# Optimization experiments

Hardware: AMD Instinct MI355X
Metric: run time of the kernel (lower is better)

The kernel has to match this reference:

```python
import math
import jax, jax.numpy as jnp
import numpy as np

P = 8; K = 9; RC = 8; FC = 768; TOPK = 2
THR = 0.2; TEMP = 0.08; DIL = 5; MIX = 0.65; OPEN = 5


def _build_bank():
    axis = np.linspace(-1.0, 1.0, K, dtype=np.float32)
    yy, xx = np.meshgrid(axis, axis, indexing='ij')
    Ls = [0.45, 0.75, 1.05]; Ws = [0.14, 0.2, 0.28]
    kernels, oris, lens, wids = [], [], [], []
    for i in range(P):
        ang = 2.0 * math.pi * i / P
        L = Ls[i % 3]; W = Ws[(i // 3) % 3]
        xr = xx * math.cos(ang) + yy * math.sin(ang)
        yr = -xx * math.sin(ang) + yy * math.cos(ang)
        taper = (1.0 - np.clip(np.abs(xr) / L, 0.0, 1.0)) ** 1.5
        core = np.exp(-0.5 * ((xr / L) ** 2 + (yr / W) ** 2))
        ridge = taper * core * np.clip(1.0 - (yr / W) ** 2, 0.0, None)
        k = ridge - ridge.mean()
        k = k / max(np.abs(k).sum(), 1e-6)
        kernels.append(k.astype(np.float32)); oris.append(ang); lens.append(L); wids.append(W)
    return (jnp.asarray(np.stack(kernels)[:, None]),
            jnp.asarray(np.array(oris, np.float32)),
            jnp.asarray(np.array(lens, np.float32)),
            jnp.asarray(np.array(wids, np.float32)))


def _conv(x, w, b, pad):
    y = jax.lax.conv_general_dilated(x, w, (1, 1), [(pad, pad), (pad, pad)],
                                     dimension_numbers=('NCHW', 'OIHW', 'NCHW'))
    return y + b[None, :, None, None]


def _avg3(x):  # torch avg_pool2d k=3,s=1,p=1 with count_include_pad=True -> sum/9
    s = jax.lax.reduce_window(x, 0.0, jax.lax.add, (1, 1, 3, 3), (1, 1, 1, 1),
                              [(0, 0), (0, 0), (1, 1), (1, 1)])
    return s / 9.0


def _maxp(x, k):
    p = k // 2
    return jax.lax.reduce_window(x, -jnp.inf, jax.lax.max, (1, 1, k, k), (1, 1, 1, 1),
                                 [(0, 0), (0, 0), (p, p), (p, p)])


def _binary_open(mask, k):
    eroded = 1.0 - _maxp(1.0 - mask, k)
    return jnp.clip(_maxp(eroded, k), 0.0, 1.0)


def _normalize(t):
    mn = t.min(axis=(-2, -1), keepdims=True)
    mx = t.max(axis=(-2, -1), keepdims=True)
    return (t - mn) / jnp.maximum(mx - mn, 1e-6)


def _gelu(x):
    return jax.nn.gelu(x, approximate=False)


def _forward(feature_map, theta, length, width, curvature, alpha, objectness,
             prototype_logits, fp1_w, fp1_b, fp2_w, fp2_b, pm1_w, pm1_b,
             pm2_w, pm2_b, proto_delta):
    bank, ori, la, wa = _build_bank()
    carrier = _gelu(_conv(_gelu(_conv(feature_map, fp1_w, fp1_b, 0)), fp2_w, fp2_b, 1))
    carrier_mean = carrier.mean(axis=1, keepdims=True)
    carrier_hp = carrier_mean - _avg3(carrier_mean)
    kernels = bank + 0.05 * proto_delta
    responses = jax.lax.conv_general_dilated(carrier_hp, kernels, (1, 1),
                                             [(K // 2, K // 2)] * 2,
                                             dimension_numbers=('NCHW', 'OIHW', 'NCHW'))
    theta_angle = jnp.tanh(theta) * math.pi  # [B,1,H,W]
    theta_score = jnp.cos(theta_angle - ori[None, :, None, None])
    length_value = jax.nn.sigmoid(length) * 0.85 + 0.25
    width_value = jax.nn.sigmoid(width) * 0.22 + 0.08
    length_score = -(length_value - la[None, :, None, None]) ** 2 / 0.08
    width_score = -(width_value - wa[None, :, None, None]) ** 2 / 0.01
    bias = prototype_logits + 1.25 * theta_score + length_score + width_score
    pw = jax.nn.softmax(bias, axis=1)  # [B,P,H,W]
    # per-pixel top-k prototype selection
    pwt = jnp.moveaxis(pw, 1, -1)  # [B,H,W,P]
    vals, idx = jax.lax.top_k(pwt, TOPK)
    sparse = (jax.nn.one_hot(idx, P, dtype=pw.dtype) * vals[..., None]).sum(axis=-2)
    sparse = sparse / jnp.maximum(sparse.sum(axis=-1, keepdims=True), 1e-6)
    pw = jnp.moveaxis(sparse, -1, 1)
    alpha_map = jax.nn.sigmoid(alpha)
    objectness_map = jax.nn.sigmoid(objectness)
    curvature_map = jnp.tanh(curvature)
    ss = (responses * pw).sum(axis=1, keepdims=True)
    ss = ss - _avg3(ss)
    density = jnp.abs(carrier).mean(axis=1, keepdims=True)
    density = density / jnp.maximum(density.mean(axis=(2, 3), keepdims=True), 1e-6)
    dx = jnp.cos(theta_angle); dy = jnp.sin(theta_angle)
    blob = _avg3(objectness_map)
    # support gating (enabled, hard-mask + opening)
    carrier_support = _normalize(_avg3(jnp.abs(carrier_hp)))
    density_support = _normalize(density)
    ev = MIX * carrier_support + (1.0 - MIX) * density_support
    gate = jax.nn.sigmoid((ev - THR) / TEMP)
    gate = _maxp(gate, DIL)
    mask = (ev >= THR).astype(feature_map.dtype)
    mask = _binary_open(mask, OPEN)
    mask = _maxp(mask, DIL)
    gate = gate * mask
    blob = blob * jax.lax.stop_gradient(gate)
    stroke_gate = alpha_map * blob * (0.7 + 0.3 * jnp.clip(density, 0.0, 2.0))
    ss = stroke_gate * ss * (1.0 + 0.15 * curvature_map)
    feats = jnp.concatenate([carrier * ss, ss, dx * ss, dy * ss, curvature_map * ss], axis=1)  # [B,RC+4,H,W]
    h = _gelu(_conv(feats, pm1_w, pm1_b, 0))
    return _conv(h, pm2_w, pm2_b, 0)  # [B,FC,H,W]


def setup_inputs() -> dict:
    key = jax.random.key(0)
    ks = jax.random.split(key, 16)
    B, H, W = 8, 64, 64
    n = lambda k, s: jax.random.normal(k, s, dtype=jnp.float32)
    return {
        'feature_map': n(ks[0], (B, FC, H, W)),
        'theta': n(ks[1], (B, 1, H, W)),
        'length': n(ks[2], (B, 1, H, W)),
        'width': n(ks[3], (B, 1, H, W)),
        'curvature': n(ks[4], (B, 1, H, W)),
        'alpha': n(ks[5], (B, 1, H, W)),
        'objectness': n(ks[6], (B, 1, H, W)),
        'prototype_logits': n(ks[7], (B, P, H, W)),
        'fp1_w': n(ks[8], (RC, FC, 1, 1)) * 0.02,
        'fp1_b': jnp.zeros((RC,), jnp.float32),
        'fp2_w': n(ks[9], (RC, RC, 3, 3)) * 0.05,
        'fp2_b': jnp.zeros((RC,), jnp.float32),
        'pm1_w': n(ks[10], (RC, RC + 4, 1, 1)) * 0.05,
        'pm1_b': jnp.zeros((RC,), jnp.float32),
        'pm2_w': n(ks[11], (FC, RC, 1, 1)) * 0.05,
        'pm2_b': jnp.zeros((FC,), jnp.float32),
        'proto_delta': n(ks[12], (P, 1, K, K)) * 0.02,
    }


def reference(feature_map, theta, length, width, curvature, alpha, objectness,
              prototype_logits, fp1_w, fp1_b, fp2_w, fp2_b, pm1_w, pm1_b,
              pm2_w, pm2_b, proto_delta):
    return _forward(feature_map, theta, length, width, curvature, alpha, objectness,
                    prototype_logits, fp1_w, fp1_b, fp2_w, fp2_b, pm1_w, pm1_b,
                    pm2_w, pm2_b, proto_delta)
```

## Files before the change

kernel.cpp:

```cpp
#include <hip/hip_runtime.h>
#include <math.h>

#define PI_F 3.14159265358979323846f

__device__ __forceinline__ float gelu_f(float x){ return 0.5f*x*(1.0f+erff(x*0.7071067811865475f)); }
__device__ __forceinline__ float sigm_f(float x){ return 1.0f/(1.0f+expf(-x)); }

typedef float nf4 __attribute__((ext_vector_type(4)));
__device__ __forceinline__ float4 nt_load4(const float4* p){
    nf4 v = __builtin_nontemporal_load((const nf4*)p);
    return make_float4(v.x, v.y, v.z, v.w);
}
__device__ __forceinline__ void nt_store4(float4* p, float4 v){
    nf4 w; w.x=v.x; w.y=v.y; w.z=v.z; w.w=v.w;
    __builtin_nontemporal_store(w, (nf4*)p);
}


__global__ void __launch_bounds__(256) k_conv1(const float* __restrict__ fm,
                        const float* __restrict__ w1, const float* __restrict__ pd,
                        float* __restrict__ part, float* __restrict__ klg){
    int chunk = blockIdx.x;
    int g = blockIdx.y;
    int tid = threadIdx.x;
    __shared__ float wl[96*8];
    __shared__ float4 comb[8][128];
    for (int i=tid;i<768;i+=256){ int c=i>>3, co=i&7; wl[i]=w1[co*768 + g*96 + c]; }
    __syncthreads();
    int b = chunk>>3;
    int f4 = tid&127, half = tid>>7;
    int q0 = ((chunk&7)<<7) + f4;
    const float4* fm4 = (const float4*)fm;
    float4 acc[8];
    #pragma unroll
    for(int co=0;co<8;co++) acc[co]=make_float4(0.f,0.f,0.f,0.f);
    int basec = b*768 + g*96 + half*48;
    for(int c=0;c<48;c++){
        float4 x = nt_load4(&fm4[(size_t)(basec+c)*1024 + q0]);
        int ch = half*48 + c;
        #pragma unroll
        for(int co=0;co<8;co++){
            float wv = wl[(ch<<3)+co];
            acc[co].x += wv*x.x; acc[co].y += wv*x.y; acc[co].z += wv*x.z; acc[co].w += wv*x.w;
        }
    }
    if(half==1){
        #pragma unroll
        for(int co=0;co<8;co++) comb[co][f4]=acc[co];
    }
    __syncthreads();
    if(half==0){
        float4* p4 = (float4*)part;
        int gq = (b<<10) + q0;
        #pragma unroll
        for(int co=0;co<8;co++){
            float4 o = comb[co][f4];
            o.x+=acc[co].x; o.y+=acc[co].y; o.z+=acc[co].z; o.w+=acc[co].w;
            p4[(size_t)((g<<3)+co)*8192 + gq] = o;
        }
    }

    if(chunk==0 && g==0){
        __shared__ float ridge[648];
        __shared__ float pmS[8], pdenS[8];
        for(int t=tid;t<648;t+=256){
            int p=t/81, idx=t-p*81;
            int i=idx/9, j=idx-i*9;
            float ay=-1.f+0.25f*(float)i;
            float ax=-1.f+0.25f*(float)j;
            float ang=2.f*PI_F*(float)p*0.125f;
            const float Ls[3]={0.45f,0.75f,1.05f};
            const float Ws[3]={0.14f,0.20f,0.28f};
            float L=Ls[p%3], Wd=Ws[(p/3)%3];
            float cs=cosf(ang), sn=sinf(ang);
            float xr=ax*cs+ay*sn;
            float yr=-ax*sn+ay*cs;
            float tp=1.f-fminf(fabsf(xr)/L,1.f);
            float taper=powf(tp,1.5f);
            float core=expf(-0.5f*((xr/L)*(xr/L)+(yr/Wd)*(yr/Wd)));
            ridge[t]=taper*core*fmaxf(1.f-(yr/Wd)*(yr/Wd),0.f);
        }
        __syncthreads();
        {
            int p=tid>>5, k=tid&31;
            float s=0.f;
            for(int e=k;e<81;e+=32) s+=ridge[p*81+e];
            for(int off=16;off>0;off>>=1) s+=__shfl_down(s,off,32);
            if(k==0) pmS[p]=s*(1.f/81.f);
        }
        __syncthreads();
        {
            int p=tid>>5, k=tid&31;
            float m=pmS[p];
            float s=0.f;
            for(int e=k;e<81;e+=32) s+=fabsf(ridge[p*81+e]-m);
            for(int off=16;off>0;off>>=1) s+=__shfl_down(s,off,32);
            if(k==0) pdenS[p]=fmaxf(s,1e-6f);
        }
        __syncthreads();
        for(int t=tid;t<648;t+=256){
            int p=t/81;
            klg[t]=(ridge[t]-pmS[p])/pdenS[p]+0.05f*pd[t];
        }
    }
}

__global__ void __launch_bounds__(256) k_conv2(const float* __restrict__ part,
    const float* __restrict__ b1, const float* __restrict__ w2, const float* __restrict__ b2,
    float* __restrict__ carrier, float* __restrict__ cm, float* __restrict__ absc,
    float* __restrict__ bpart){
    __shared__ float t1T[8][256];
    __shared__ float w2s[576];
    __shared__ float b1s[8];
    __shared__ float sumS[2][128];
    __shared__ float saS[2][128];
    __shared__ float rS[256], rMn[256], rMx[256];
    int tid=threadIdx.x, bl=blockIdx.x;
    int b=bl>>5, band=bl&31, y0=band<<1;
    for(int i=tid;i<576;i+=256) w2s[i]=w2[i];
    if(tid<8) b1s[tid]=b1[tid];
    __syncthreads();
    for(int j=tid;j<2048;j+=256){
        int co=j>>8, pos=j&255, r=pos>>6, x=pos&63;
        int gy=y0-1+r;
        float v=0.f;
        if(gy>=0 && gy<64){
            int px=(b<<12)+(gy<<6)+x;
            float s=0.f;
            #pragma unroll
            for(int g=0;g<8;g++) s+=part[(size_t)((g<<3)+co)*32768+px];
            v=gelu_f(s+b1s[co]);
        }
        t1T[co][pos]=v;
    }
    __syncthreads();
    int px=tid&127, half=tid>>7;
    int ly=px>>6, x=px&63, gy=y0+ly;
    float acc[4];
    #pragma unroll
    for(int qq=0;qq<4;qq++) acc[qq]=b2[half*4+qq];
    for(int ci=0;ci<8;ci++){
        #pragma unroll
        for(int dy=-1;dy<=1;dy++){
            int tr=ly+1+dy;
            #pragma unroll
            for(int dx=-1;dx<=1;dx++){
                int xx=x+dx;
                float v=(xx>=0&&xx<64)?t1T[ci][tr*64+xx]:0.f;
                int ti=(dy+1)*3+(dx+1);
                #pragma unroll
                for(int qq=0;qq<4;qq++) acc[qq]+=v*w2s[((half*4+qq)*8+ci)*9+ti];
            }
        }
    }
    float s4=0.f, sa4=0.f;
    #pragma unroll
    for(int qq=0;qq<4;qq++){
        float cv=gelu_f(acc[qq]);
        carrier[((size_t)((b<<3)+half*4+qq)<<12)+(gy<<6)+x]=cv;
        s4+=cv; sa4+=fabsf(cv);
    }
    sumS[half][px]=s4; saS[half][px]=sa4;
    __syncthreads();
    float aS=0.f, aMn=1e30f, aMx=-1e30f;
    if(half==0){
        float cmv=(sumS[0][px]+sumS[1][px])*0.125f;
        float av =(saS[0][px]+saS[1][px])*0.125f;
        int gp=(b<<12)+(gy<<6)+x;
        cm[gp]=cmv;
        absc[gp]=av;
        aS=av; aMn=av; aMx=av;
    }
    rS[tid]=aS; rMn[tid]=aMn; rMx[tid]=aMx;
    __syncthreads();
    for(int st=128;st>0;st>>=1){
        if(tid<st){
            rS[tid]+=rS[tid+st];
            rMn[tid]=fminf(rMn[tid],rMn[tid+st]);
            rMx[tid]=fmaxf(rMx[tid],rMx[tid+st]);
        }
        __syncthreads();
    }
    if(tid==0){
        bpart[bl*8+0]=rS[0];
        bpart[bl*8+3]=rMn[0];
        bpart[bl*8+4]=rMx[0];
    }
}

__global__ void __launch_bounds__(256) k_resp(const float* __restrict__ cm,
    const float* __restrict__ klg, const float* __restrict__ theta,
    const float* __restrict__ length, const float* __restrict__ width,
    const float* __restrict__ plog,
    float* __restrict__ csraw, float* __restrict__ ss0, float* __restrict__ bpart){
    __shared__ float cmT[768];
    __shared__ float chpT[640];
    __shared__ float klS[648];
    __shared__ float mg[128][8];
    __shared__ float rMn[256], rMx[256];
    int tid=threadIdx.x, bl=blockIdx.x;
    int b=bl>>5, band=bl&31, y0=band<<1;
    for(int i=tid;i<648;i+=256) klS[i]=klg[i];
    for(int j=tid;j<768;j+=256){
        int r=j>>6, x=j&63;
        int gy=y0-5+r;
        cmT[j]=(gy>=0&&gy<64)?cm[(b<<12)+(gy<<6)+x]:0.f;
    }
    __syncthreads();
    for(int j=tid;j<640;j+=256){
        int rh=j>>6, x=j&63;
        int gy=y0-4+rh;
        float v=0.f;
        if(gy>=0&&gy<64){
            float s=0.f;
            #pragma unroll
            for(int dy=-1;dy<=1;dy++){
                #pragma unroll
                for(int dx=-1;dx<=1;dx++){
                    int xx=x+dx;
                    if(xx>=0&&xx<64) s+=cmT[(rh+1+dy)*64+xx];
                }
            }
            v=cmT[(rh+1)*64+x]-s*(1.f/9.f);
        }
        chpT[j]=v;
    }
    __syncthreads();
    int px=tid&127, half=tid>>7;
    int ly=px>>6, x=px&63, gy=y0+ly;
    int gp=(b<<12)+(gy<<6)+x;
    float acc[4];
    #pragma unroll
    for(int qq=0;qq<4;qq++) acc[qq]=0.f;
    float cs=0.f;
    for(int dy=-4;dy<=4;dy++){
        int lr=ly+dy+4;
        for(int dx=-4;dx<=4;dx++){
            int xx=x+dx;
            float v=(xx>=0&&xx<64)?chpT[lr*64+xx]:0.f;
            int ti=(dy+4)*9+(dx+4);
            #pragma unroll
            for(int qq=0;qq<4;qq++) acc[qq]+=v*klS[(half*4+qq)*81+ti];
            if(half==0 && dy>=-1&&dy<=1&&dx>=-1&&dx<=1) cs+=fabsf(v);
        }
    }
    float ta=tanhf(theta[gp])*PI_F;
    float lv=sigm_f(length[gp])*0.85f+0.25f;
    float wv=sigm_f(width[gp])*0.22f+0.08f;
    const float Ls[3]={0.45f,0.75f,1.05f};
    const float Ws[3]={0.14f,0.20f,0.28f};
    int pp=(gy<<6)+x;
    float m1=-1e30f,m2=-1e30f,r1v=0.f,r2v=0.f;
    #pragma unroll
    for(int qq=0;qq<4;qq++){
        int q=half*4+qq;
        float ang=2.f*PI_F*(float)q*0.125f;
        float la=Ls[q%3], wa=Ws[(q/3)%3];
        float bias=plog[((size_t)((b<<3)+q)<<12)+pp]
                 +1.25f*cosf(ta-ang)
                 -(lv-la)*(lv-la)*(1.f/0.08f)
                 -(wv-wa)*(wv-wa)*(1.f/0.01f);
        if(bias>m1){m2=m1;r2v=r1v;m1=bias;r1v=acc[qq];}
        else if(bias>m2){m2=bias;r2v=acc[qq];}
    }
    mg[px][half*4+0]=m1; mg[px][half*4+1]=r1v;
    mg[px][half*4+2]=m2; mg[px][half*4+3]=r2v;
    __syncthreads();
    float cMn=1e30f, cMx=-1e30f;
    if(half==0){
        float m1a=mg[px][0], r1a=mg[px][1], m2a=mg[px][2], r2a=mg[px][3];
        float m1b=mg[px][4], r1b=mg[px][5], m2b=mg[px][6], r2b=mg[px][7];
        float M1,R1,M2,R2;
        if(m1b>m1a){ M1=m1b;R1=r1b; if(m2b>m1a){M2=m2b;R2=r2b;} else {M2=m1a;R2=r1a;} }
        else       { M1=m1a;R1=r1a; if(m1b>m2a){M2=m1b;R2=r1b;} else {M2=m2a;R2=r2a;} }
        float e2=expf(M2-M1);
        float inv=1.0f/(1.0f+e2);
        ss0[gp]=R1*inv + R2*e2*inv;
        float csv=cs*(1.f/9.f);
        csraw[gp]=csv;
        cMn=csv; cMx=csv;
    }
    rMn[tid]=cMn; rMx[tid]=cMx;
    __syncthreads();
    for(int st=128;st>0;st>>=1){
        if(tid<st){
            rMn[tid]=fminf(rMn[tid],rMn[tid+st]);
            rMx[tid]=fmaxf(rMx[tid],rMx[tid+st]);
        }
        __syncthreads();
    }
    if(tid==0){
        bpart[bl*8+1]=rMn[0];
        bpart[bl*8+2]=rMx[0];
    }
}

__global__ void __launch_bounds__(256) k_gate(const float* __restrict__ csraw,
    const float* __restrict__ absc, const float* __restrict__ objn,
    const float* __restrict__ alpha, const float* __restrict__ bpart,
    float* __restrict__ sg){
    __shared__ float evT[1280];
    __shared__ float gmT[1280];
    __shared__ float eT[1024];
    __shared__ float m1T[768];
    __shared__ float obT[640];
    __shared__ float red5[5];
    int blk=blockIdx.x, tid=threadIdx.x;
    int b=blk>>3, y0=(blk&7)<<3;
    if(tid==0){
        float sm=0.f, cmn=1e30f, cmx=-1e30f, amn=1e30f, amx=-1e30f;
        for(int j=0;j<32;j++){
            const float* bp=&bpart[(b*32+j)*8];
            sm+=bp[0];
            cmn=fminf(cmn,bp[1]); cmx=fmaxf(cmx,bp[2]);
            amn=fminf(amn,bp[3]); amx=fmaxf(amx,bp[4]);
        }
        float den=fmaxf(sm*(1.0f/4096.0f),1e-6f);
        red5[0]=den; red5[1]=cmn; red5[2]=cmx; red5[3]=amn/den; red5[4]=amx/den;
    }
    __syncthreads();
    float den=red5[0], cmn=red5[1], dmn=red5[3];
    float cinv = 1.0f/fmaxf(red5[2]-cmn,1e-6f);
    float dinv = 1.0f/fmaxf(red5[4]-dmn,1e-6f);
    for(int j=tid;j<1280;j+=256){
        int r=j>>6, x=j&63; int gy=y0-6+r;
        float ev=0.f;
        if(gy>=0&&gy<64){
            int gp=(b<<12)+(gy<<6)+x;
            float cs=(csraw[gp]-cmn)*cinv;
            float d=absc[gp]/den;
            ev=0.65f*cs+0.35f*((d-dmn)*dinv);
        }
        evT[j]=ev;
        gmT[j]=sigm_f((ev-0.2f)*(1.0f/0.08f));
    }
    for(int j=tid;j<640;j+=256){
        int r=j>>6,x=j&63; int gy=y0-1+r;
        obT[j]=(gy>=0&&gy<64)?sigm_f(objn[(b<<12)+(gy<<6)+x]):0.f;
    }
    __syncthreads();
    for(int j=tid;j<1024;j+=256){
        int r=j>>6,x=j&63; int gy=y0-4+r;
        float m=0.f;
        if(gy>=0&&gy<64){
            m=1.f;
            for(int dy=-2;dy<=2;dy++){int yy=gy+dy; if(yy<0||yy>=64)continue;
                int lr=yy-(y0-6);
                for(int dx=-2;dx<=2;dx++){int xx=x+dx; if(xx<0||xx>=64)continue;
                    if(evT[(lr<<6)+xx]<0.2f) m=0.f;}}
        }
        eT[j]=m;
    }
    __syncthreads();
    for(int j=tid;j<768;j+=256){
        int r=j>>6,x=j&63; int gy=y0-2+r;
        float m=0.f;
        if(gy>=0&&gy<64){
            m=-1e30f;
            for(int dy=-2;dy<=2;dy++){int yy=gy+dy; if(yy<0||yy>=64)continue;
                int lr=yy-(y0-4);
                for(int dx=-2;dx<=2;dx++){int xx=x+dx; if(xx<0||xx>=64)continue;
                    m=fmaxf(m,eT[(lr<<6)+xx]);}}
        }
        m1T[j]=m;
    }
    __syncthreads();
    for(int k=0;k<2;k++){
        int p=tid+(k<<8);
        int ly=p>>6, x=p&63; int gy=y0+ly;
        int gp=(b<<12)+(gy<<6)+x;
        float m2=-1e30f, gx=-1e30f;
        for(int dy=-2;dy<=2;dy++){int yy=gy+dy; if(yy<0||yy>=64)continue;
            int lr1=yy-(y0-2), lr2=yy-(y0-6);
            for(int dx=-2;dx<=2;dx++){int xx=x+dx; if(xx<0||xx>=64)continue;
                m2=fmaxf(m2,m1T[(lr1<<6)+xx]);
                gx=fmaxf(gx,gmT[(lr2<<6)+xx]);}}
        float s=0.f;
        for(int dy=-1;dy<=1;dy++){int yy=gy+dy; if(yy<0||yy>=64)continue;
            int lr=yy-(y0-1);
            for(int dx=-1;dx<=1;dx++){int xx=x+dx; if(xx<0||xx>=64)continue;
                s+=obT[(lr<<6)+xx];}}
        float blob=s*(1.0f/9.0f);
        float gate=gx*m2;
        float d=absc[gp]/den;
        sg[gp]=sigm_f(alpha[gp])*blob*gate*(0.7f+0.3f*fminf(fmaxf(d,0.f),2.f));
    }
}

__global__ void __launch_bounds__(256) k_out(const float* __restrict__ ss0,
    const float* __restrict__ sg, const float* __restrict__ theta,
    const float* __restrict__ curv, const float* __restrict__ carrier,
    const float* __restrict__ w3, const float* __restrict__ b3,
    const float* __restrict__ w4, const float* __restrict__ b4,
    float* __restrict__ out){
    __shared__ float hS[8][64];
    __shared__ float w4s[768*8];
    __shared__ float b4s[768];
    __shared__ float wl[96];
    __shared__ float bl3[8];
    int tid=threadIdx.x;
    int bln=blockIdx.x;
    for(int i=tid;i<6144;i+=256) w4s[i]=w4[i];
    for(int i=tid;i<768;i+=256) b4s[i]=b4[i];
    if(tid<96) wl[tid]=w3[tid];
    if(tid<8) bl3[tid]=b3[tid];
    __syncthreads();

    if(tid<64){
        int gp=bln*64+tid;
        int b=gp>>12, p=gp&4095, y=p>>6, x=p&63;
        const float* base = ss0 + (b<<12);
        float s=0.f;
        for(int dy=-1;dy<=1;dy++){int yy=y+dy; if(yy<0||yy>=64)continue;
            for(int dx=-1;dx<=1;dx++){int xx=x+dx;if(xx<0||xx>=64)continue;
                s+=base[(yy<<6)+xx];}}
        float ss1 = base[p]-s*(1.0f/9.0f);
        float cu = tanhf(curv[gp]);
        float ssv = sg[gp]*ss1*(1.0f+0.15f*cu);
        float ta = tanhf(theta[gp])*PI_F;
        float dxv=cosf(ta), dyv=sinf(ta);
        float car[8];
        #pragma unroll
        for(int ci=0;ci<8;ci++) car[ci]=carrier[((size_t)((b<<3)+ci)<<12)+p];
        #pragma unroll
        for(int co=0;co<8;co++){
            const float* w=&wl[co*12];
            float t = w[8] + w[9]*dxv + w[10]*dyv + w[11]*cu;
            #pragma unroll
            for(int ci=0;ci<8;ci++) t += w[ci]*car[ci];
            hS[co][tid] = gelu_f(bl3[co] + ssv*t);
        }
    }
    __syncthreads();

    int px4 = tid&15;
    int cg = tid>>4;
    int q0 = bln*16 + px4;
    int b = q0>>10;
    int ql = q0 & 1023;
    float4 hv[8];
    #pragma unroll
    for(int ci=0;ci<8;ci++) hv[ci]=*(const float4*)&hS[ci][px4<<2];
    float4* o4=(float4*)out;
    for(int k=0;k<48;k++){
        int co=cg*48+k;
        float bb=b4s[co];
        float4 o=make_float4(bb,bb,bb,bb);
        const float* w=&w4s[co<<3];
        #pragma unroll
        for(int ci=0;ci<8;ci++){
            float wv=w[ci];
            o.x+=wv*hv[ci].x; o.y+=wv*hv[ci].y; o.z+=wv*hv[ci].z; o.w+=wv*hv[ci].w;
        }
        nt_store4(&o4[(size_t)(b*768+co)*1024 + ql], o);
    }
}

extern "C" void kernel_launch(void* const* d_in, const int* in_sizes, int n_in,
                              void* d_out, int out_size, void* d_ws, size_t ws_size,
                              hipStream_t stream) {
    const float* fm     =(const float*)d_in[0];
    const float* theta  =(const float*)d_in[1];
    const float* length =(const float*)d_in[2];
    const float* width  =(const float*)d_in[3];
    const float* curv   =(const float*)d_in[4];
    const float* alpha  =(const float*)d_in[5];
    const float* objn   =(const float*)d_in[6];
    const float* plog   =(const float*)d_in[7];
    const float* fp1w   =(const float*)d_in[8];
    const float* fp1b   =(const float*)d_in[9];
    const float* fp2w   =(const float*)d_in[10];
    const float* fp2b   =(const float*)d_in[11];
    const float* pm1w   =(const float*)d_in[12];
    const float* pm1b   =(const float*)d_in[13];
    const float* pm2w   =(const float*)d_in[14];
    const float* pm2b   =(const float*)d_in[15];
    const float* pdelta =(const float*)d_in[16];

    float* ws=(float*)d_ws;
    float* part    = ws;
    float* carrier = part + 2097152;
    float* absc    = carrier + 262144;
    float* csraw   = absc + 32768;
    float* ss0     = csraw + 32768;
    float* sg      = ss0 + 32768;
    float* cm      = sg + 32768;
    float* bpart   = cm + 32768;
    float* klg     = bpart + 2048;
    float* out     = (float*)d_out;

    k_conv1<<<dim3(64,8), 256, 0, stream>>>(fm, fp1w, pdelta, part, klg);
    k_conv2<<<256, 256, 0, stream>>>(part, fp1b, fp2w, fp2b, carrier, cm, absc, bpart);
    k_resp <<<256, 256, 0, stream>>>(cm, klg, theta, length, width, plog,
                                     csraw, ss0, bpart);
    k_gate <<<64, 256, 0, stream>>>(csraw, absc, objn, alpha, bpart, sg);
    k_out  <<<512, 256, 0, stream>>>(ss0, sg, theta, curv, carrier,
                                     pm1w, pm1b, pm2w, pm2b, out);
}
```

Before: 284.5 us.

## Split conv2 and resp into one-row blocks with wave-shuffle reductions

k_conv2 and k_resp now give each block a single output row instead of two, doubling the grid to 512 blocks. Each thread handles 2 output channels or prototypes instead of 4, and the block-wide shared-memory reductions become 64-lane wavefront shuffles. bpart grows to hold 64 partials per batch, and k_gate sums over them. The aim is more parallelism and fewer barriers, at the cost of more halo rows being recomputed (part loads, gelu, high-pass) per output row. An unroll hint is also added to the conv1 channel loop.

After: 281.7 us. About the same (-1.0%).

```diff
diff --git a/kernel.cpp b/kernel.cpp
--- a/kernel.cpp
+++ b/kernel.cpp
@@ -35,6 +35,7 @@
     #pragma unroll
     for(int co=0;co<8;co++) acc[co]=make_float4(0.f,0.f,0.f,0.f);
     int basec = b*768 + g*96 + half*48;
+    #pragma unroll 4
     for(int c=0;c<48;c++){
         float4 x = nt_load4(&fm4[(size_t)(basec+c)*1024 + q0]);
         int ch = half*48 + c;
@@ -109,82 +110,74 @@
     const float* __restrict__ b1, const float* __restrict__ w2, const float* __restrict__ b2,
     float* __restrict__ carrier, float* __restrict__ cm, float* __restrict__ absc,
     float* __restrict__ bpart){
-    __shared__ float t1T[8][256];
+    __shared__ float t1T[8][3][64];
     __shared__ float w2s[576];
     __shared__ float b1s[8];
-    __shared__ float sumS[2][128];
-    __shared__ float saS[2][128];
-    __shared__ float rS[256], rMn[256], rMx[256];
+    __shared__ float sumS[4][64];
+    __shared__ float saS[4][64];
     int tid=threadIdx.x, bl=blockIdx.x;
-    int b=bl>>5, band=bl&31, y0=band<<1;
+    int b=bl>>6, y=bl&63;
     for(int i=tid;i<576;i+=256) w2s[i]=w2[i];
     if(tid<8) b1s[tid]=b1[tid];
     __syncthreads();
-    for(int j=tid;j<2048;j+=256){
-        int co=j>>8, pos=j&255, r=pos>>6, x=pos&63;
-        int gy=y0-1+r;
+    for(int j=tid;j<1536;j+=256){
+        int ci=j/192, rem=j-ci*192, r=rem>>6, x=rem&63;
+        int gy=y-1+r;
         float v=0.f;
         if(gy>=0 && gy<64){
             int px=(b<<12)+(gy<<6)+x;
             float s=0.f;
             #pragma unroll
-            for(int g=0;g<8;g++) s+=part[(size_t)((g<<3)+co)*32768+px];
-            v=gelu_f(s+b1s[co]);
-        }
-        t1T[co][pos]=v;
-    }
-    __syncthreads();
-    int px=tid&127, half=tid>>7;
-    int ly=px>>6, x=px&63, gy=y0+ly;
-    float acc[4];
+            for(int g=0;g<8;g++) s+=part[(size_t)((g<<3)+ci)*32768+px];
+            v=gelu_f(s+b1s[ci]);
+        }
+        t1T[ci][r][x]=v;
+    }
+    __syncthreads();
+    int x=tid&63, cg=tid>>6;
+    float acc[2];
     #pragma unroll
-    for(int qq=0;qq<4;qq++) acc[qq]=b2[half*4+qq];
+    for(int qq=0;qq<2;qq++) acc[qq]=b2[cg*2+qq];
     for(int ci=0;ci<8;ci++){
         #pragma unroll
-        for(int dy=-1;dy<=1;dy++){
-            int tr=ly+1+dy;
+        for(int r=0;r<3;r++){
             #pragma unroll
             for(int dx=-1;dx<=1;dx++){
                 int xx=x+dx;
-                float v=(xx>=0&&xx<64)?t1T[ci][tr*64+xx]:0.f;
-                int ti=(dy+1)*3+(dx+1);
+                float v=(xx>=0&&xx<64)?t1T[ci][r][xx]:0.f;
+                int ti=r*3+(dx+1);
                 #pragma unroll
-                for(int qq=0;qq<4;qq++) acc[qq]+=v*w2s[((half*4+qq)*8+ci)*9+ti];
+                for(int qq=0;qq<2;qq++) acc[qq]+=v*w2s[(((cg*2+qq)*8+ci)*9)+ti];
             }
         }
     }
-    float s4=0.f, sa4=0.f;
+    float s2=0.f, sa2=0.f;
     #pragma unroll
-    for(int qq=0;qq<4;qq++){
+    for(int qq=0;qq<2;qq++){
         float cv=gelu_f(acc[qq]);
-        carrier[((size_t)((b<<3)+half*4+qq)<<12)+(gy<<6)+x]=cv;
-        s4+=cv; sa4+=fabsf(cv);
-    }
-    sumS[half][px]=s4; saS[half][px]=sa4;
-    __syncthreads();
-    float aS=0.f, aMn=1e30f, aMx=-1e30f;
-    if(half==0){
-        float cmv=(sumS[0][px]+sumS[1][px])*0.125f;
-        float av =(saS[0][px]+saS[1][px])*0.125f;
-        int gp=(b<<12)+(gy<<6)+x;
+        carrier[((size_t)((b<<3)+cg*2+qq)<<12)+(y<<6)+x]=cv;
+        s2+=cv; sa2+=fabsf(cv);
+    }
+    sumS[cg][x]=s2; saS[cg][x]=sa2;
+    __syncthreads();
+    if(cg==0){
+        float cmv=(sumS[0][x]+sumS[1][x]+sumS[2][x]+sumS[3][x])*0.125f;
+        float av =(saS[0][x]+saS[1][x]+saS[2][x]+saS[3][x])*0.125f;
+        int gp=(b<<12)+(y<<6)+x;
         cm[gp]=cmv;
         absc[gp]=av;
-        aS=av; aMn=av; aMx=av;
-    }
-    rS[tid]=aS; rMn[tid]=aMn; rMx[tid]=aMx;
-    __syncthreads();
-    for(int st=128;st>0;st>>=1){
-        if(tid<st){
-            rS[tid]+=rS[tid+st];
-            rMn[tid]=fminf(rMn[tid],rMn[tid+st]);
-            rMx[tid]=fmaxf(rMx[tid],rMx[tid+st]);
-        }
-        __syncthreads();
-    }
-    if(tid==0){
-        bpart[bl*8+0]=rS[0];
-        bpart[bl*8+3]=rMn[0];
-        bpart[bl*8+4]=rMx[0];
+        float s=av, mn=av, mx=av;
+        #pragma unroll
+        for(int off=32;off>0;off>>=1){
+            s += __shfl_down(s,off);
+            mn = fminf(mn,__shfl_down(mn,off));
+            mx = fmaxf(mx,__shfl_down(mx,off));
+        }
+        if(x==0){
+            bpart[bl*8+0]=s;
+            bpart[bl*8+3]=mn;
+            bpart[bl*8+4]=mx;
+        }
     }
 }
 
@@ -193,32 +186,31 @@
     const float* __restrict__ length, const float* __restrict__ width,
     const float* __restrict__ plog,
     float* __restrict__ csraw, float* __restrict__ ss0, float* __restrict__ bpart){
-    __shared__ float cmT[768];
-    __shared__ float chpT[640];
+    __shared__ float cmT[704];
+    __shared__ float chpT[576];
     __shared__ float klS[648];
-    __shared__ float mg[128][8];
-    __shared__ float rMn[256], rMx[256];
+    __shared__ float mg[64][16];
     int tid=threadIdx.x, bl=blockIdx.x;
-    int b=bl>>5, band=bl&31, y0=band<<1;
+    int b=bl>>6, y=bl&63;
     for(int i=tid;i<648;i+=256) klS[i]=klg[i];
-    for(int j=tid;j<768;j+=256){
+    for(int j=tid;j<704;j+=256){
         int r=j>>6, x=j&63;
-        int gy=y0-5+r;
+        int gy=y-5+r;
         cmT[j]=(gy>=0&&gy<64)?cm[(b<<12)+(gy<<6)+x]:0.f;
     }
     __syncthreads();
-    for(int j=tid;j<640;j+=256){
+    for(int j=tid;j<576;j+=256){
         int rh=j>>6, x=j&63;
-        int gy=y0-4+rh;
+        int gy=y-4+rh;
         float v=0.f;
         if(gy>=0&&gy<64){
             float s=0.f;
             #pragma unroll
-            for(int dy=-1;dy<=1;dy++){
+            for(int dy=0;dy<3;dy++){
                 #pragma unroll
                 for(int dx=-1;dx<=1;dx++){
                     int xx=x+dx;
-                    if(xx>=0&&xx<64) s+=cmT[(rh+1+dy)*64+xx];
+                    if(xx>=0&&xx<64) s+=cmT[(rh+dy)*64+xx];
                 }
             }
             v=cmT[(rh+1)*64+x]-s*(1.f/9.f);
@@ -226,22 +218,19 @@
         chpT[j]=v;
     }
     __syncthreads();
-    int px=tid&127, half=tid>>7;
-    int ly=px>>6, x=px&63, gy=y0+ly;
-    int gp=(b<<12)+(gy<<6)+x;
-    float acc[4];
-    #pragma unroll
-    for(int qq=0;qq<4;qq++) acc[qq]=0.f;
+    int x=tid&63, qg=tid>>6;
+    int gp=(b<<12)+(y<<6)+x;
+    float acc[2]={0.f,0.f};
     float cs=0.f;
     for(int dy=-4;dy<=4;dy++){
-        int lr=ly+dy+4;
+        int lr=dy+4;
         for(int dx=-4;dx<=4;dx++){
             int xx=x+dx;
             float v=(xx>=0&&xx<64)?chpT[lr*64+xx]:0.f;
-            int ti=(dy+4)*9+(dx+4);
-            #pragma unroll
-            for(int qq=0;qq<4;qq++) acc[qq]+=v*klS[(half*4+qq)*81+ti];
-            if(half==0 && dy>=-1&&dy<=1&&dx>=-1&&dx<=1) cs+=fabsf(v);
+            int ti=lr*9+(dx+4);
+            acc[0]+=v*klS[(qg*2)*81+ti];
+            acc[1]+=v*klS[(qg*2+1)*81+ti];
+            if(qg==0 && dy>=-1&&dy<=1&&dx>=-1&&dx<=1) cs+=fabsf(v);
         }
     }
     float ta=tanhf(theta[gp])*PI_F;
@@ -249,49 +238,51 @@
     float wv=sigm_f(width[gp])*0.22f+0.08f;
     const float Ls[3]={0.45f,0.75f,1.05f};
     const float Ws[3]={0.14f,0.20f,0.28f};
-    int pp=(gy<<6)+x;
-    float m1=-1e30f,m2=-1e30f,r1v=0.f,r2v=0.f;
+    int pp=(y<<6)+x;
+    float bias[2];
     #pragma unroll
-    for(int qq=0;qq<4;qq++){
-        int q=half*4+qq;
+    for(int qq=0;qq<2;qq++){
+        int q=qg*2+qq;
         float ang=2.f*PI_F*(float)q*0.125f;
         float la=Ls[q%3], wa=Ws[(q/3)%3];
-        float bias=plog[((size_t)((b<<3)+q)<<12)+pp]
-                 +1.25f*cosf(ta-ang)
-                 -(lv-la)*(lv-la)*(1.f/0.08f)
-                 -(wv-wa)*(wv-wa)*(1.f/0.01f);
-        if(bias>m1){m2=m1;r2v=r1v;m1=bias;r1v=acc[qq];}
-        else if(bias>m2){m2=bias;r2v=acc[qq];}
-    }
-    mg[px][half*4+0]=m1; mg[px][half*4+1]=r1v;
-    mg[px][half*4+2]=m2; mg[px][half*4+3]=r2v;
-    __syncthreads();
-    float cMn=1e30f, cMx=-1e30f;
-    if(half==0){
-        float m1a=mg[px][0], r1a=mg[px][1], m2a=mg[px][2], r2a=mg[px][3];
-        float m1b=mg[px][4], r1b=mg[px][5], m2b=mg[px][6], r2b=mg[px][7];
-        float M1,R1,M2,R2;
-        if(m1b>m1a){ M1=m1b;R1=r1b; if(m2b>m1a){M2=m2b;R2=r2b;} else {M2=m1a;R2=r1a;} }
-        else       { M1=m1a;R1=r1a; if(m1b>m2a){M2=m1b;R2=r1b;} else {M2=m2a;R2=r2a;} }
+        bias[qq]=plog[((size_t)((b<<3)+q)<<12)+pp]
+               +1.25f*cosf(ta-ang)
+               -(lv-la)*(lv-la)*(1.f/0.08f)
+               -(wv-wa)*(wv-wa)*(1.f/0.01f);
+    }
+    float m1,r1,m2,r2;
+    if(bias[1]>bias[0]){ m1=bias[1];r1=acc[1]; m2=bias[0];r2=acc[0]; }
+    else               { m1=bias[0];r1=acc[0]; m2=bias[1];r2=acc[1]; }
+    mg[x][qg*4+0]=m1; mg[x][qg*4+1]=r1; mg[x][qg*4+2]=m2; mg[x][qg*4+3]=r2;
+    __syncthreads();
+    if(qg==0){
+        float M1=mg[x][0],R1=mg[x][1],M2=mg[x][2],R2=mg[x][3];
+        #pragma unroll
+        for(int g=1;g<4;g++){
+            float m1b=mg[x][g*4],r1b=mg[x][g*4+1],m2b=mg[x][g*4+2],r2b=mg[x][g*4+3];
+            if(m1b>M1){
+                float nM2,nR2;
+                if(m2b>M1){nM2=m2b;nR2=r2b;} else {nM2=M1;nR2=R1;}
+                M1=m1b;R1=r1b;M2=nM2;R2=nR2;
+            } else if(m1b>M2){
+                M2=m1b;R2=r1b;
+            }
+        }
         float e2=expf(M2-M1);
         float inv=1.0f/(1.0f+e2);
         ss0[gp]=R1*inv + R2*e2*inv;
         float csv=cs*(1.f/9.f);
         csraw[gp]=csv;
-        cMn=csv; cMx=csv;
-    }
-    rMn[tid]=cMn; rMx[tid]=cMx;
-    __syncthreads();
-    for(int st=128;st>0;st>>=1){
-        if(tid<st){
-            rMn[tid]=fminf(rMn[tid],rMn[tid+st]);
-            rMx[tid]=fmaxf(rMx[tid],rMx[tid+st]);
-        }
-        __syncthreads();
-    }
-    if(tid==0){
-        bpart[bl*8+1]=rMn[0];
-        bpart[bl*8+2]=rMx[0];
+        float mn=csv, mx=csv;
+        #pragma unroll
+        for(int off=32;off>0;off>>=1){
+            mn=fminf(mn,__shfl_down(mn,off));
+            mx=fmaxf(mx,__shfl_down(mx,off));
+        }
+        if(x==0){
+            bpart[bl*8+1]=mn;
+            bpart[bl*8+2]=mx;
+        }
     }
 }
 
@@ -309,8 +300,8 @@
     int b=blk>>3, y0=(blk&7)<<3;
     if(tid==0){
         float sm=0.f, cmn=1e30f, cmx=-1e30f, amn=1e30f, amx=-1e30f;
-        for(int j=0;j<32;j++){
-            const float* bp=&bpart[(b*32+j)*8];
+        for(int j=0;j<64;j++){
+            const float* bp=&bpart[(b*64+j)*8];
             sm+=bp[0];
             cmn=fminf(cmn,bp[1]); cmx=fmaxf(cmx,bp[2]);
             amn=fminf(amn,bp[3]); amx=fmaxf(amx,bp[4]);
@@ -486,12 +477,12 @@
     float* sg      = ss0 + 32768;
     float* cm      = sg + 32768;
     float* bpart   = cm + 32768;
-    float* klg     = bpart + 2048;
+    float* klg     = bpart + 4096;
     float* out     = (float*)d_out;
 
     k_conv1<<<dim3(64,8), 256, 0, stream>>>(fm, fp1w, pdelta, part, klg);
-    k_conv2<<<256, 256, 0, stream>>>(part, fp1b, fp2w, fp2b, carrier, cm, absc, bpart);
-    k_resp <<<256, 256, 0, stream>>>(cm, klg, theta, length, width, plog,
+    k_conv2<<<512, 256, 0, stream>>>(part, fp1b, fp2w, fp2b, carrier, cm, absc, bpart);
+    k_resp <<<512, 256, 0, stream>>>(cm, klg, theta, length, width, plog,
                                      csraw, ss0, bpart);
     k_gate <<<64, 256, 0, stream>>>(csraw, absc, objn, alpha, bpart, sg);
     k_out  <<<512, 256, 0, stream>>>(ss0, sg, theta, curv, carrier,
```
